# Performance work log

Measured on AMD Instinct MI355X. Metric: run time of the kernel, lower is better.

The kernel has to match this reference:

```python
import jax, jax.numpy as jnp
import numpy as np

B, T, N, E = 64, 500, 21, 210
IN_DIM, HID, OUT_DIM = 1, 128, 1


def gcn_norm(edge_index, edge_weight, num_nodes):
    # PyG gcn_norm: add self loops (weight 1), deg over target nodes, symmetric normalization.
    src, dst = edge_index[0], edge_index[1]
    loop = jnp.arange(num_nodes)
    src = jnp.concatenate([src, loop])
    dst = jnp.concatenate([dst, loop])
    ew = jnp.concatenate([edge_weight, jnp.ones((num_nodes,), edge_weight.dtype)])
    deg = jnp.zeros((num_nodes,), edge_weight.dtype).at[dst].add(ew)
    dinv = jnp.where(deg > 0, deg ** -0.5, 0.0)
    norm = dinv[src] * ew * dinv[dst]
    # Dense N x N (N=21, tiny) normalized adjacency; out[i] = sum_j A[i, j] x[j].
    return jnp.zeros((num_nodes, num_nodes), edge_weight.dtype).at[dst, src].add(norm)


def _forward(edge_index, x, edge_weight, Wz_1, bz_1, lzw_1, lzb_1, Wr_1, br_1, lrw_1, lrb_1, Wh_1, bh_1, lhw_1, lhb_1, Wz_2, bz_2, lzw_2, lzb_2, Wr_2, br_2, lrw_2, lrb_2, Wh_2, bh_2, lhw_2, lhb_2, cls_w, cls_b):
    A = gcn_norm(edge_index, edge_weight, N)

    def gcn(X, W, b):  # X: (B, N, F)
        return jnp.einsum("ij,bjf->bif", A, X @ W) + b

    def cell(X, H, Wz, bz, lzw, lzb, Wr, br, lrw, lrb, Wh, bh, lhw, lhb):
        Z = jax.nn.sigmoid(jnp.concatenate([gcn(X, Wz, bz), H], -1) @ lzw + lzb)
        R = jax.nn.sigmoid(jnp.concatenate([gcn(X, Wr, br), H], -1) @ lrw + lrb)
        Ht = jnp.tanh(jnp.concatenate([gcn(X, Wh, bh), H * R], -1) @ lhw + lhb)
        return Z * H + (1.0 - Z) * Ht

    def step(carry, x_t):  # x_t: (B, N)
        H1, H2 = carry
        X = x_t[..., None]  # (B, N, 1)
        H1 = cell(X, H1, Wz_1, bz_1, lzw_1, lzb_1, Wr_1, br_1, lrw_1, lrb_1, Wh_1, bh_1, lhw_1, lhb_1)
        H2 = cell(H1, H2, Wz_2, bz_2, lzw_2, lzb_2, Wr_2, br_2, lrw_2, lrb_2, Wh_2, bh_2, lhw_2, lhb_2)
        return (H1, H2), H2.mean(axis=1)  # mean over nodes -> (B, HID)

    H0 = jnp.zeros((x.shape[0], N, HID), x.dtype)
    _, outs = jax.lax.scan(step, (H0, H0), jnp.moveaxis(x, 1, 0))  # outs: (T, B, HID)
    seq_out = outs.mean(axis=0)  # mean over time (== mean over nodes then time in original)
    return seq_out @ cls_w + cls_b  # (B, OUT_DIM)


def setup_inputs():
    key = jax.random.key(0)
    ks = list(jax.random.split(key, 20))
    kit = iter(ks)

    def nrm(shape, scale=0.05):
        return jax.random.normal(next(kit), shape, jnp.float32) * scale

    inp = {}
    inp["x"] = jax.random.normal(next(kit), (B, T, N), jnp.float32)
    inp["edge_index"] = jax.random.randint(next(kit), (2, E), 0, N)
    inp["edge_weight"] = jax.random.uniform(next(kit), (E,), jnp.float32)
    for tag, in_dim in (("1", IN_DIM), ("2", HID)):
        for g in "zrh":
            inp[f"W{g}_{tag}"] = nrm((in_dim, HID))
            inp[f"b{g}_{tag}"] = jnp.zeros((HID,), jnp.float32)
            inp[f"l{g}w_{tag}"] = nrm((2 * HID, HID))
            inp[f"l{g}b_{tag}"] = jnp.zeros((HID,), jnp.float32)
    inp["cls_w"] = nrm((HID, OUT_DIM))
    inp["cls_b"] = jnp.zeros((OUT_DIM,), jnp.float32)
    return inp


def reference(x, edge_index, edge_weight, Wz_1, bz_1, lzw_1, lzb_1, Wr_1, br_1, lrw_1, lrb_1, Wh_1, bh_1, lhw_1, lhb_1, Wz_2, bz_2, lzw_2, lzb_2, Wr_2, br_2, lrw_2, lrb_2, Wh_2, bh_2, lhw_2, lhb_2, cls_w, cls_b):
    return _forward(edge_index, x, edge_weight, Wz_1, bz_1, lzw_1, lzb_1, Wr_1, br_1, lrw_1, lrb_1, Wh_1, bh_1, lhw_1, lhb_1, Wz_2, bz_2, lzw_2, lzb_2, Wr_2, br_2, lrw_2, lrb_2, Wh_2, bh_2, lhw_2, lhb_2, cls_w, cls_b)
```

## Files before the change

### kernel.cpp

```cpp
#include <hip/hip_runtime.h>
#include <hip/hip_bf16.h>


#define NN 21
#define NROW 24
#define HID 128
#define TSTEPS 500
#define EDGES 210
#define RPT 6

#define WS_A     0
#define WS_VEC   1600
#define WS_LZR1  3200
#define WS_LH1   36000
#define WS_WE2   52400
#define WS_LZR2  101600
#define WS_LH2   134400
#define WS_FLAGS 150784
#define WS_RING  154880
#define RING_SLOT 3072

#define WAVE_SYNC() asm volatile("s_waitcnt lgkmcnt(0)" ::: "memory")
#define VM_SYNC()   asm volatile("s_waitcnt vmcnt(0)" ::: "memory")

typedef float v2f __attribute__((ext_vector_type(2)));

__device__ __forceinline__ v2f lo2(float4 w) { v2f v = {w.x, w.y}; return v; }
__device__ __forceinline__ v2f hi2(float4 w) { v2f v = {w.z, w.w}; return v; }
__device__ __forceinline__ void pkf(v2f& acc, float s, v2f w) {
    v2f ss = {s, s};
    acc = __builtin_elementwise_fma(ss, w, acc);
}
__device__ __forceinline__ float sigmoidf(float v) {
    return 1.0f / (1.0f + expf(-v));
}
__device__ __forceinline__ void dc_store(float* p, float v) {
    asm volatile("global_store_dword %0, %1, off sc0 sc1" :: "v"(p), "v"(v) : "memory");
}

__global__ void build_A(const int* __restrict__ ei, const float* __restrict__ ew,
                        float* __restrict__ Aout) {
    __shared__ double deg[NN];
    __shared__ double dinv[NN];
    __shared__ double Asm[NN * NN];
    int t = threadIdx.x;
    for (int k = t; k < NN * NN; k += blockDim.x) Asm[k] = 0.0;
    if (t < NN) deg[t] = 1.0;
    __syncthreads();
    if (t == 0) {
        for (int e = 0; e < EDGES; e++) deg[ei[EDGES + e]] += (double)ew[e];
        for (int i = 0; i < NN; i++) dinv[i] = deg[i] > 0.0 ? 1.0 / sqrt(deg[i]) : 0.0;
        for (int e = 0; e < EDGES; e++) {
            int s = ei[e], d = ei[EDGES + e];
            Asm[d * NN + s] += dinv[s] * (double)ew[e] * dinv[d];
        }
        for (int i = 0; i < NN; i++) Asm[i * NN + i] += dinv[i] * dinv[i];
    }
    __syncthreads();
    for (int k = t; k < NROW * NN; k += blockDim.x)
        Aout[k] = (k < NN * NN) ? (float)Asm[k] : 0.0f;
}

// ... 41 lines not shown
    double a0 = 0, a1 = 0, a2 = 0, a3 = 0;
    for (int m = 0; m < 128; m++) {
        double w0 = (double)W[k * 128 + m];
        double w1 = (double)W[(k + 1) * 128 + m];
        a0 += w0 * (double)L[m * 128 + f0];
        a1 += w0 * (double)L[m * 128 + f0 + 64];
        a2 += w1 * (double)L[m * 128 + f0];
        a3 += w1 * (double)L[m * 128 + f0 + 64];
    }
    out[t] = make_float4((float)a0, (float)a1, (float)a2, (float)a3);
}

__global__ void make_vecs(const float* __restrict__ Wz1, const float* __restrict__ Wr1,
                          const float* __restrict__ Wh1,
                          const float* __restrict__ bz1, const float* __restrict__ br1,
                          const float* __restrict__ bh1,
                          const float* __restrict__ lzw1, const float* __restrict__ lrw1,
                          const float* __restrict__ lhw1,
                          const float* __restrict__ lzb1, const float* __restrict__ lrb1,
                          const float* __restrict__ lhb1,
                          const float* __restrict__ bz2, const float* __restrict__ br2,
                          const float* __restrict__ bh2,
                          const float* __restrict__ lzw2, const float* __restrict__ lrw2,
                          const float* __restrict__ lhw2,
                          const float* __restrict__ lzb2, const float* __restrict__ lrb2,
                          const float* __restrict__ lhb2,
                          float* __restrict__ out) {
    int t = blockIdx.x * blockDim.x + threadIdx.x;
    if (t >= 9 * 128) return;
    int v = t >> 7, f = t & 127;
    double acc = 0.0;
    if (v < 3) {
        const float* W = (v == 0) ? Wz1 : (v == 1) ? Wr1 : Wh1;
        const float* L = (v == 0) ? lzw1 : (v == 1) ? lrw1 : lhw1;
        for (int m = 0; m < 128; m++) acc += (double)W[m] * (double)L[m * 128 + f];
    } else if (v < 6) {
        int g = v - 3;
        const float* bb = (g == 0) ? bz1 : (g == 1) ? br1 : bh1;
        const float* L  = (g == 0) ? lzw1 : (g == 1) ? lrw1 : lhw1;
        const float* lb = (g == 0) ? lzb1 : (g == 1) ? lrb1 : lhb1;
        for (int m = 0; m < 128; m++) acc += (double)bb[m] * (double)L[m * 128 + f];
        acc += (double)lb[f];
    } else {
        int g = v - 6;
        const float* bb = (g == 0) ? bz2 : (g == 1) ? br2 : bh2;
        const float* L  = (g == 0) ? lzw2 : (g == 1) ? lrw2 : lhw2;
        const float* lb = (g == 0) ? lzb2 : (g == 1) ? lrb2 : lhb2;
        for (int m = 0; m < 128; m++) acc += (double)bb[m] * (double)L[m * 128 + f];
        acc += (double)lb[f];
    }
    out[t] = (float)acc;
}

__global__ __launch_bounds__(256, 1) void tgcn_split(
    const float* __restrict__ x, float* __restrict__ ws,
    const float* __restrict__ cls_w, const float* __restrict__ cls_b,
    float* __restrict__ out, int rdepth)
{
    const int bid = blockIdx.x;
    const bool roleA = (bid < 64);
    const int b  = bid & 63;
    const int t  = threadIdx.x;
    const int f0 = t & 63;
    const int f1 = f0 + 64;
    const int gw = __builtin_amdgcn_readfirstlane(t >> 6);
    const int iA = gw * RPT;
    const int nreal = (iA + RPT <= NN) ? RPT : (NN - iA);
    const int dmask = rdepth - 1;

    unsigned* fwdp  = (unsigned*)(ws + WS_FLAGS) + b * 32;
    unsigned* backp = (unsigned*)(ws + WS_FLAGS) + 2048 + b * 32;
    float* ringB = ws + WS_RING + (size_t)b * ((size_t)rdepth * RING_SLOT);

    __shared__ __align__(16) float sH1[2][NROW * HID];
    __shared__ __align__(16) float sHR1[NROW * HID];
    __shared__ __align__(16) float sH1B[2][NROW * HID];
    __shared__ __align__(16) float sH2[NROW * HID];
    __shared__ __align__(16) float sHR2[NROW * HID];
    __shared__ __align__(16) float sAH[NROW * HID];
    __shared__ float sA[NROW * NN];
    __shared__ float sax[2][NROW];
    __shared__ double sred[4][HID];

    const float*  vecs = ws + WS_VEC;
    const float4* Lzr1 = (const float4*)(ws + WS_LZR1);
    const float4* Lh1  = (const float4*)(ws + WS_LH1);
    const float4* We2  = (const float4*)(ws + WS_WE2);
    const float4* Lzr2 = (const float4*)(ws + WS_LZR2);
    const float4* Lh2  = (const float4*)(ws + WS_LH2);

    const float4* HR1v = (const float4*)sHR1;
    const float4* HR2v = (const float4*)sHR2;
    const float4* AHv  = (const float4*)sAH;
    const float4* H2v  = (const float4*)sH2;

    for (int k = t; k < 2 * NROW * HID; k += 256) {
        ((float*)sH1)[k] = 0.0f;
        ((float*)sH1B)[k] = 0.0f;
    }
    for (int k = t; k < NROW * HID; k += 256) {
        sH2[k] = 0.0f; sHR1[k] = 0.0f; sHR2[k] = 0.0f; sAH[k] = 0.0f;
    }
    for (int k = t; k < NROW * NN; k += 256) sA[k] = ws[WS_A + k];

    const v2f wz1v = {vecs[f0],        vecs[f1]};
    const v2f wr1v = {vecs[128 + f0],  vecs[128 + f1]};
    const v2f wh1v = {vecs[256 + f0],  vecs[256 + f1]};
    const v2f cz1v = {vecs[384 + f0],  vecs[384 + f1]};
    const v2f cr1v = {vecs[512 + f0],  vecs[512 + f1]};
    const v2f ch1v = {vecs[640 + f0],  vecs[640 + f1]};
    const v2f cz2v = {vecs[768 + f0],  vecs[768 + f1]};
    const v2f cr2v = {vecs[896 + f0],  vecs[896 + f1]};
    const v2f ch2v = {vecs[1024 + f0], vecs[1024 + f1]};

    __syncthreads();

    if (roleA) {
        const float* xb = x + (size_t)b * (TSTEPS * NN);
        if (t < NROW) {
            float a0s = 0.0f, a1s = 0.0f;
            for (int j = 0; j < NN; j++) {
                a0s = fmaf(sA[t * NN + j], xb[j], a0s);
                a1s = fmaf(sA[t * NN + j], xb[NN + j], a1s);
            }
            sax[0][t] = a0s;
            sax[1][t] = a1s;
        }
        __syncthreads();

        for (int s = 0; s < TSTEPS; s++) {
            if (t == 0 && s >= rdepth) {
                while (__hip_atomic_load(backp, __ATOMIC_RELAXED,
                                         __HIP_MEMORY_SCOPE_AGENT) < (unsigned)(s - rdepth + 1))
                    __builtin_amdgcn_s_sleep(2);
            }
            __syncthreads();

            {
                const float* H1rd = sH1[(s + 1) & 1];
                float*       H1wr = sH1[s & 1];
                const float4* H1c = (const float4*)H1rd;
                float* g = ringB + (s & dmask) * RING_SLOT;
                float axp[RPT];
                #pragma unroll
                for (int r = 0; r < RPT; r++) axp[r] = sax[s & 1][iA + r];
                v2f az[RPT], ar[RPT];
                #pragma unroll
                for (int r = 0; r < RPT; r++) {
                    az[r] = __builtin_elementwise_fma((v2f){axp[r], axp[r]}, wz1v, cz1v);
                    ar[r] = __builtin_elementwise_fma((v2f){axp[r], axp[r]}, wr1v, cr1v);
                }
                #pragma unroll 2
                for (int c = 0; c < 32; ++c) {
                    const float4 wz0 = Lzr1[c * 256 + f0];
                    const float4 wz1 = Lzr1[c * 256 + 64 + f0];
                    const float4 wr0 = Lzr1[c * 256 + 128 + f0];
                    const float4 wr1 = Lzr1[c * 256 + 192 + f0];
                    #pragma unroll
                    for (int r = 0; r < RPT; r++) {
                        const float4 h = H1c[(iA + r) * 32 + c];
                        pkf(az[r], h.x, lo2(wz0)); pkf(az[r], h.y, hi2(wz0));
                        pkf(az[r], h.z, lo2(wz1)); pkf(az[r], h.w, hi2(wz1));
                        pkf(ar[r], h.x, lo2(wr0)); pkf(ar[r], h.y, hi2(wr0));
                        pkf(ar[r], h.z, lo2(wr1)); pkf(ar[r], h.w, hi2(wr1));
                    }
                }
                v2f zg[RPT], h1c[RPT];
                #pragma unroll
                for (int r = 0; r < RPT; r++) {
                    zg[r].x = sigmoidf(az[r].x);
                    zg[r].y = sigmoidf(az[r].y);
                    const float r0 = sigmoidf(ar[r].x);
                    const float r1 = sigmoidf(ar[r].y);
                    h1c[r].x = H1rd[(iA + r) * HID + f0];
                    h1c[r].y = H1rd[(iA + r) * HID + f1];
                    sHR1[(iA + r) * HID + f0] = h1c[r].x * r0;
                    sHR1[(iA + r) * HID + f1] = h1c[r].y * r1;
                }
                WAVE_SYNC();
                v2f ah[RPT];
                #pragma unroll
                for (int r = 0; r < RPT; r++)
                    ah[r] = __builtin_elementwise_fma((v2f){axp[r], axp[r]}, wh1v, ch1v);
                #pragma unroll 2
                for (int c = 0; c < 32; ++c) {
                    const float4 wh0 = Lh1[c * 128 + f0];
                    const float4 wh1 = Lh1[c * 128 + 64 + f0];
                    #pragma unroll
                    for (int r = 0; r < RPT; r++) {
                        const float4 q = HR1v[(iA + r) * 32 + c];
                        pkf(ah[r], q.x, lo2(wh0)); pkf(ah[r], q.y, hi2(wh0));
                        pkf(ah[r], q.z, lo2(wh1)); pkf(ah[r], q.w, hi2(wh1));
                    }
                }
                #pragma unroll
                for (int r = 0; r < RPT; r++) {
                    const int row = iA + r;
                    const float n0 = fmaf(zg[r].x, h1c[r].x, (1.0f - zg[r].x) * tanhf(ah[r].x));
                    const float n1 = fmaf(zg[r].y, h1c[r].y, (1.0f - zg[r].y) * tanhf(ah[r].y));
                    H1wr[row * HID + f0] = n0;
                    H1wr[row * HID + f1] = n1;
                    dc_store(g + row * HID + f0, n0);
                    dc_store(g + row * HID + f1, n1);
                }
            }
            if (t < NROW && s + 2 < TSTEPS) {
                const float* xt = xb + (size_t)(s + 2) * NN;
                float a = 0.0f;
                for (int j = 0; j < NN; j++) a = fmaf(sA[t * NN + j], xt[j], a);
                sax[(s + 2) & 1][t] = a;
            }
            VM_SYNC();
            __syncthreads();
            if (t == 0)
                __hip_atomic_store(fwdp, (unsigned)(s + 1), __ATOMIC_RELAXED,
                                   __HIP_MEMORY_SCOPE_AGENT);
        }
        return;
    }

    double oacc0 = 0.0, oacc1 = 0.0;
    v2f ph[RPT], z2[RPT], h2c[RPT];

    auto l2_p5 = [&]() {
        #pragma unroll 2
        for (int c = 0; c < 32; ++c) {
            const float4 lh0 = Lh2[c * 128 + f0];
            const float4 lh1 = Lh2[c * 128 + 64 + f0];
            #pragma unroll
            for (int r = 0; r < RPT; r++) {
                const float4 q = HR2v[(iA + r) * 32 + c];
                pkf(ph[r], q.x, lo2(lh0)); pkf(ph[r], q.y, hi2(lh0));
                pkf(ph[r], q.z, lo2(lh1)); pkf(ph[r], q.w, hi2(lh1));
            }
        }
        #pragma unroll
        for (int r = 0; r < RPT; r++) {
            const float m0 = fmaf(z2[r].x, h2c[r].x, (1.0f - z2[r].x) * tanhf(ph[r].x));
            const float m1 = fmaf(z2[r].y, h2c[r].y, (1.0f - z2[r].y) * tanhf(ph[r].y));
            sH2[(iA + r) * HID + f0] = m0;
            sH2[(iA + r) * HID + f1] = m1;
            if (r < nreal) {
                oacc0 += (double)m0;
                oacc1 += (double)m1;
            }
        }
    };

    {
        if (t == 0) {
            while (__hip_atomic_load(fwdp, __ATOMIC_RELAXED,
                                     __HIP_MEMORY_SCOPE_AGENT) < 1u)
                __builtin_amdgcn_s_sleep(2);
        }
        __syncthreads();
        const float4* gs = (const float4*)(ringB + 0 * RING_SLOT);
        const float4* p0 = gs + t;
        const float4* p1 = gs + t + 256;
        const float4* p2 = gs + t + 512;
        float4 v0, v1, v2;
        asm volatile(
            "global_load_dwordx4 %0, %3, off sc0 sc1\n\t"
            "global_load_dwordx4 %1, %4, off sc0 sc1\n\t"
            "global_load_dwordx4 %2, %5, off sc0 sc1\n\t"
            "s_waitcnt vmcnt(0)"
            : "=v"(v0), "=v"(v1), "=v"(v2)
            : "v"(p0), "v"(p1), "v"(p2)
            : "memory");
        float4* sB = (float4*)sH1B[0];
        sB[t] = v0; sB[t + 256] = v1; sB[t + 512] = v2;
        __syncthreads();
        if (t == 0)
            __hip_atomic_store(backp, 1u, __ATOMIC_RELAXED,
                               __HIP_MEMORY_SCOPE_AGENT);
    }

    for (int k = 0; k < TSTEPS; k++) {
        const float* H1k = sH1B[k & 1];
        {
            v2f aa[RPT];
            #pragma unroll
            for (int r = 0; r < RPT; r++) aa[r] = (v2f){0.0f, 0.0f};
            #pragma unroll 3
            for (int j = 0; j < NN; j++) {
                const v2f hj = {H1k[j * HID + f0], H1k[j * HID + f1]};
                #pragma unroll
                for (int r = 0; r < RPT; r++) {
                    const float arj = sA[(iA + r) * NN + j];
                    aa[r] = __builtin_elementwise_fma((v2f){arj, arj}, hj, aa[r]);
                }
            }
            #pragma unroll
            for (int r = 0; r < RPT; r++) {
                sAH[(iA + r) * HID + f0] = aa[r].x;
                sAH[(iA + r) * HID + f1] = aa[r].y;
            }
        }
        WAVE_SYNC();
        const bool pf = (k + 1 < TSTEPS);
        float4 v0, v1, v2;
        if (pf) {
            if (t == 0) {
                while (__hip_atomic_load(fwdp, __ATOMIC_RELAXED,
                                         __HIP_MEMORY_SCOPE_AGENT) < (unsigned)(k + 2))
                    __builtin_amdgcn_s_sleep(2);
            }
            __syncthreads();
            const float4* gs = (const float4*)(ringB + ((k + 1) & dmask) * RING_SLOT);
            const float4* p0 = gs + t;
            const float4* p1 = gs + t + 256;
            const float4* p2 = gs + t + 512;
            asm volatile(
                "global_load_dwordx4 %0, %3, off sc0 sc1\n\t"
                "global_load_dwordx4 %1, %4, off sc0 sc1\n\t"
                "global_load_dwordx4 %2, %5, off sc0 sc1"
                : "=v"(v0), "=v"(v1), "=v"(v2)
                : "v"(p0), "v"(p1), "v"(p2)
                : "memory");
        }
        {
            v2f pz[RPT], pr[RPT];
            #pragma unroll
            for (int r = 0; r < RPT; r++) { pz[r] = cz2v; pr[r] = cr2v; ph[r] = ch2v; }
            for (int c = 0; c < 32; ++c) {
                const float4 wz0 = We2[c * 384 + f0];
                const float4 wz1 = We2[c * 384 + 64 + f0];
                const float4 wr0 = We2[c * 384 + 128 + f0];
                const float4 wr1 = We2[c * 384 + 192 + f0];
                const float4 wh0 = We2[c * 384 + 256 + f0];
                const float4 wh1 = We2[c * 384 + 320 + f0];
                const float4 lz0 = Lzr2[c * 256 + f0];
                const float4 lz1 = Lzr2[c * 256 + 64 + f0];
                const float4 lr0 = Lzr2[c * 256 + 128 + f0];
                const float4 lr1 = Lzr2[c * 256 + 192 + f0];
                #pragma unroll
                for (int r = 0; r < RPT; r++) {
                    const float4 a = AHv[(iA + r) * 32 + c];
                    const float4 q = H2v[(iA + r) * 32 + c];
                    pkf(pz[r], a.x, lo2(wz0)); pkf(pz[r], a.y, hi2(wz0));
                    pkf(pz[r], a.z, lo2(wz1)); pkf(pz[r], a.w, hi2(wz1));
                    pkf(pz[r], q.x, lo2(lz0)); pkf(pz[r], q.y, hi2(lz0));
                    pkf(pz[r], q.z, lo2(lz1)); pkf(pz[r], q.w, hi2(lz1));
                    pkf(pr[r], a.x, lo2(wr0)); pkf(pr[r], a.y, hi2(wr0));
                    pkf(pr[r], a.z, lo2(wr1)); pkf(pr[r], a.w, hi2(wr1));
                    pkf(pr[r], q.x, lo2(lr0)); pkf(pr[r], q.y, hi2(lr0));
                    pkf(pr[r], q.z, lo2(lr1)); pkf(pr[r], q.w, hi2(lr1));
                    pkf(ph[r], a.x, lo2(wh0)); pkf(ph[r], a.y, hi2(wh0));
                    pkf(ph[r], a.z, lo2(wh1)); pkf(ph[r], a.w, hi2(wh1));
                }
            }
            #pragma unroll
            for (int r = 0; r < RPT; r++) {
                z2[r].x = sigmoidf(pz[r].x);
                z2[r].y = sigmoidf(pz[r].y);
                const float r20 = sigmoidf(pr[r].x);
                const float r21 = sigmoidf(pr[r].y);
                h2c[r].x = sH2[(iA + r) * HID + f0];
                h2c[r].y = sH2[(iA + r) * HID + f1];
                sHR2[(iA + r) * HID + f0] = h2c[r].x * r20;
                sHR2[(iA + r) * HID + f1] = h2c[r].y * r21;
            }
        }
        WAVE_SYNC();
        if (pf) {
            asm volatile("s_waitcnt vmcnt(0)" ::: "memory");
            __builtin_amdgcn_sched_barrier(0);
            float4* sB = (float4*)sH1B[(k + 1) & 1];
            sB[t] = v0; sB[t + 256] = v1; sB[t + 512] = v2;
            __syncthreads();
            if (t == 0)
                __hip_atomic_store(backp, (unsigned)(k + 2), __ATOMIC_RELAXED,
                                   __HIP_MEMORY_SCOPE_AGENT);
        }
        l2_p5();
    }

    sred[gw][f0] = oacc0;
    sred[gw][f1] = oacc1;
    __syncthreads();
    if (t < HID) {
        double s = 0.0;
        for (int gg = 0; gg < 4; gg++) s += sred[gg][t];
        sred[0][t] = (s / (double)(TSTEPS * NN)) * (double)cls_w[t];
    }
    __syncthreads();
    if (t < 64) {
        double v = ((double*)sred)[t] + ((double*)sred)[t + 64];
        for (int off = 32; off; off >>= 1) v += __shfl_down(v, off, 64);
        if (t == 0) out[b] = (float)(v + (double)cls_b[0]);
    }
}

#define NTHREADS 512
__global__ __launch_bounds__(NTHREADS, 1) void tgcn_main(
    const float* __restrict__ x, const float* __restrict__ ws,
    const float* __restrict__ cls_w, const float* __restrict__ cls_b,
    float* __restrict__ out)
{
    const int b  = blockIdx.x;
    const int t  = threadIdx.x;
    const bool isA = (t < 256);
    const int lt = t & 255;
    const int f0 = lt & 63;
    const int f1 = f0 + 64;
    const int gw = __builtin_amdgcn_readfirstlane(lt >> 6);
    const int iA = gw * RPT;
    const int nreal = (iA + RPT <= NN) ? RPT : (NN - iA);

    __shared__ __align__(16) float sH1[2][NROW * HID];
    __shared__ __align__(16) float sH2[NROW * HID];
    __shared__ __align__(16) float sHR1[NROW * HID];
    __shared__ __align__(16) float sHR2[NROW * HID];
    __shared__ __align__(16) float sAH[NROW * HID];
    __shared__ float sA[NROW * NN];
    __shared__ float sax[2][NROW];
    __shared__ double sred[4][HID];

    const float*  vecs = ws + WS_VEC;
    const float4* Lzr1 = (const float4*)(ws + WS_LZR1);
    const float4* Lh1  = (const float4*)(ws + WS_LH1);
    const float4* We2  = (const float4*)(ws + WS_WE2);
    const float4* Lzr2 = (const float4*)(ws + WS_LZR2);
    const float4* Lh2  = (const float4*)(ws + WS_LH2);

    const float4* H2v  = (const float4*)sH2;
    const float4* HR1v = (const float4*)sHR1;
    const float4* HR2v = (const float4*)sHR2;
    const float4* AHv  = (const float4*)sAH;

    for (int k = t; k < 2 * NROW * HID; k += NTHREADS) ((float*)sH1)[k] = 0.0f;
    for (int k = t; k < NROW * HID; k += NTHREADS) sH2[k] = 0.0f;
    for (int k = t; k < NROW * NN; k += NTHREADS) sA[k] = ws[WS_A + k];

    const v2f wz1v = {vecs[f0],        vecs[f1]};
    const v2f wr1v = {vecs[128 + f0],  vecs[128 + f1]};
    const v2f wh1v = {vecs[256 + f0],  vecs[256 + f1]};
// ... 212 lines not shown
    const float* x    = (const float*)d_in[0];
    const int*   ei   = (const int*)  d_in[1];
    const float* ew   = (const float*)d_in[2];
    const float* Wz1  = (const float*)d_in[3];
    const float* bz1  = (const float*)d_in[4];
    const float* lzw1 = (const float*)d_in[5];
    const float* lzb1 = (const float*)d_in[6];
    const float* Wr1  = (const float*)d_in[7];
    const float* br1  = (const float*)d_in[8];
    const float* lrw1 = (const float*)d_in[9];
    const float* lrb1 = (const float*)d_in[10];
    const float* Wh1  = (const float*)d_in[11];
    const float* bh1  = (const float*)d_in[12];
    const float* lhw1 = (const float*)d_in[13];
    const float* lhb1 = (const float*)d_in[14];
    const float* Wz2  = (const float*)d_in[15];
    const float* bz2  = (const float*)d_in[16];
    const float* lzw2 = (const float*)d_in[17];
    const float* lzb2 = (const float*)d_in[18];
    const float* Wr2  = (const float*)d_in[19];
    const float* br2  = (const float*)d_in[20];
    const float* lrw2 = (const float*)d_in[21];
    const float* lrb2 = (const float*)d_in[22];
    const float* Wh2  = (const float*)d_in[23];
    const float* bh2  = (const float*)d_in[24];
    const float* lhw2 = (const float*)d_in[25];
    const float* lhb2 = (const float*)d_in[26];
    const float* clsw = (const float*)d_in[27];
    const float* clsb = (const float*)d_in[28];

    float* ws   = (float*)d_ws;
    float* outp = (float*)d_out;

    build_A<<<1, 64, 0, stream>>>(ei, ew, ws + WS_A);
    pack_bot<<<32, 256, 0, stream>>>(lzw1, lrw1, (float4*)(ws + WS_LZR1), 2);
    pack_bot<<<16, 256, 0, stream>>>(lhw1, lhw1, (float4*)(ws + WS_LH1), 1);
    pack_bot<<<32, 256, 0, stream>>>(lzw2, lrw2, (float4*)(ws + WS_LZR2), 2);
    pack_bot<<<16, 256, 0, stream>>>(lhw2, lhw2, (float4*)(ws + WS_LH2), 1);
    make_weff2<<<48, 256, 0, stream>>>(Wz2, Wr2, Wh2, lzw2, lrw2, lhw2,
                                       (float4*)(ws + WS_WE2));
    make_vecs<<<5, 256, 0, stream>>>(Wz1, Wr1, Wh1, bz1, br1, bh1,
                                     lzw1, lrw1, lhw1, lzb1, lrb1, lhb1,
                                     bz2, br2, bh2, lzw2, lrw2, lhw2,
                                     lzb2, lrb2, lhb2, ws + WS_VEC);

    const size_t need4 = (size_t)(WS_RING + 64 * 4 * RING_SLOT) * sizeof(float);
    const size_t need2 = (size_t)(WS_RING + 64 * 2 * RING_SLOT) * sizeof(float);
    int rdepth = 0;
    if (ws_size >= need4)      rdepth = 4;
    else if (ws_size >= need2) rdepth = 2;

    if (rdepth) {
        init_flags<<<16, 256, 0, stream>>>((unsigned*)(ws + WS_FLAGS));
        tgcn_split<<<128, 256, 0, stream>>>(x, ws, clsw, clsb, outp, rdepth);
    } else {
        tgcn_main<<<64, NTHREADS, 0, stream>>>(x, ws, clsw, clsb, outp);
    }
}
```

Measured before the change: 10.06 ms.

## Double split-kernel block size to 512 threads with 3 rows per thread

Raises tgcn_split from 256 to 512 threads per block. Each wave now splits its lanes into two row groups of 3 rows, and each wave covers half of the feature columns, so every thread works on 3 node rows instead of 6. The goal is more parallelism per CU and shorter per-thread serial FMA chains for the recurrent step. The cost is extra block-wide __syncthreads barriers, since cross-wave LDS data dependencies now exist, plus a shuffle-based final reduction and reworked ring-buffer loads.

After: 12.66 ms. +25.9%, slower.

```diff
diff --git a/kernel.cpp b/kernel.cpp
--- a/kernel.cpp
+++ b/kernel.cpp
@@ -8,6 +8,7 @@
 #define TSTEPS 500
 #define EDGES 210
 #define RPT 6
+#define RPTS 3
 
 #define WS_A     0
 #define WS_VEC   1600
@@ -155,7 +156,7 @@
     out[t] = (float)acc;
 }
 
-__global__ __launch_bounds__(256, 1) void tgcn_split(
+__global__ __launch_bounds__(512, 1) void tgcn_split(
     const float* __restrict__ x, float* __restrict__ ws,
     const float* __restrict__ cls_w, const float* __restrict__ cls_b,
     float* __restrict__ out, int rdepth)
@@ -164,11 +165,15 @@
     const bool roleA = (bid < 64);
     const int b  = bid & 63;
     const int t  = threadIdx.x;
-    const int f0 = t & 63;
+    const int w  = __builtin_amdgcn_readfirstlane(t >> 6);
+    const int lane = t & 63;
+    const int half = w & 1;
+    const int wp = w >> 1;
+    const int rg = wp * 2 + (lane >> 5);
+    const int iA = rg * RPTS;
+    const int f0 = (lane & 31) + half * 32;
     const int f1 = f0 + 64;
-    const int gw = __builtin_amdgcn_readfirstlane(t >> 6);
-    const int iA = gw * RPT;
-    const int nreal = (iA + RPT <= NN) ? RPT : (NN - iA);
+    const int nreal = (iA + RPTS <= NN) ? RPTS : ((NN > iA) ? (NN - iA) : 0);
     const int dmask = rdepth - 1;
 
     unsigned* fwdp  = (unsigned*)(ws + WS_FLAGS) + b * 32;
@@ -197,14 +202,14 @@
     const float4* AHv  = (const float4*)sAH;
     const float4* H2v  = (const float4*)sH2;
 
-    for (int k = t; k < 2 * NROW * HID; k += 256) {
+    for (int k = t; k < 2 * NROW * HID; k += 512) {
         ((float*)sH1)[k] = 0.0f;
         ((float*)sH1B)[k] = 0.0f;
     }
-    for (int k = t; k < NROW * HID; k += 256) {
+    for (int k = t; k < NROW * HID; k += 512) {
         sH2[k] = 0.0f; sHR1[k] = 0.0f; sHR2[k] = 0.0f; sAH[k] = 0.0f;
     }
-    for (int k = t; k < NROW * NN; k += 256) sA[k] = ws[WS_A + k];
+    for (int k = t; k < NROW * NN; k += 512) sA[k] = ws[WS_A + k];
 
     const v2f wz1v = {vecs[f0],        vecs[f1]};
     const v2f wr1v = {vecs[128 + f0],  vecs[128 + f1]};
@@ -244,12 +249,12 @@
                 float*       H1wr = sH1[s & 1];
                 const float4* H1c = (const float4*)H1rd;
                 float* g = ringB + (s & dmask) * RING_SLOT;
-                float axp[RPT];
-                #pragma unroll
-                for (int r = 0; r < RPT; r++) axp[r] = sax[s & 1][iA + r];
-                v2f az[RPT], ar[RPT];
-                #pragma unroll
-                for (int r = 0; r < RPT; r++) {
+                float axp[RPTS];
+                #pragma unroll
+                for (int r = 0; r < RPTS; r++) axp[r] = sax[s & 1][iA + r];
+                v2f az[RPTS], ar[RPTS];
+                #pragma unroll
+                for (int r = 0; r < RPTS; r++) {
                     az[r] = __builtin_elementwise_fma((v2f){axp[r], axp[r]}, wz1v, cz1v);
                     ar[r] = __builtin_elementwise_fma((v2f){axp[r], axp[r]}, wr1v, cr1v);
                 }
@@ -260,7 +265,7 @@
                     const float4 wr0 = Lzr1[c * 256 + 128 + f0];
                     const float4 wr1 = Lzr1[c * 256 + 192 + f0];
                     #pragma unroll
-                    for (int r = 0; r < RPT; r++) {
+                    for (int r = 0; r < RPTS; r++) {
                         const float4 h = H1c[(iA + r) * 32 + c];
                         pkf(az[r], h.x, lo2(wz0)); pkf(az[r], h.y, hi2(wz0));
                         pkf(az[r], h.z, lo2(wz1)); pkf(az[r], h.w, hi2(wz1));
@@ -268,9 +273,9 @@
                         pkf(ar[r], h.z, lo2(wr1)); pkf(ar[r], h.w, hi2(wr1));
                     }
                 }
-                v2f zg[RPT], h1c[RPT];
-                #pragma unroll
-                for (int r = 0; r < RPT; r++) {
+                v2f zg[RPTS], h1c[RPTS];
+                #pragma unroll
+                for (int r = 0; r < RPTS; r++) {
                     zg[r].x = sigmoidf(az[r].x);
                     zg[r].y = sigmoidf(az[r].y);
                     const float r0 = sigmoidf(ar[r].x);
@@ -281,23 +286,24 @@
                     sHR1[(iA + r) * HID + f1] = h1c[r].y * r1;
                 }
                 WAVE_SYNC();
-                v2f ah[RPT];
-                #pragma unroll
-                for (int r = 0; r < RPT; r++)
+                __syncthreads();
+                v2f ah[RPTS];
+                #pragma unroll
+                for (int r = 0; r < RPTS; r++)
                     ah[r] = __builtin_elementwise_fma((v2f){axp[r], axp[r]}, wh1v, ch1v);
                 #pragma unroll 2
                 for (int c = 0; c < 32; ++c) {
                     const float4 wh0 = Lh1[c * 128 + f0];
                     const float4 wh1 = Lh1[c * 128 + 64 + f0];
                     #pragma unroll
-                    for (int r = 0; r < RPT; r++) {
+                    for (int r = 0; r < RPTS; r++) {
                         const float4 q = HR1v[(iA + r) * 32 + c];
                         pkf(ah[r], q.x, lo2(wh0)); pkf(ah[r], q.y, hi2(wh0));
                         pkf(ah[r], q.z, lo2(wh1)); pkf(ah[r], q.w, hi2(wh1));
                     }
                 }
                 #pragma unroll
-                for (int r = 0; r < RPT; r++) {
+                for (int r = 0; r < RPTS; r++) {
                     const int row = iA + r;
                     const float n0 = fmaf(zg[r].x, h1c[r].x, (1.0f - zg[r].x) * tanhf(ah[r].x));
                     const float n1 = fmaf(zg[r].y, h1c[r].y, (1.0f - zg[r].y) * tanhf(ah[r].y));
@@ -323,7 +329,7 @@
     }
 
     double oacc0 = 0.0, oacc1 = 0.0;
-    v2f ph[RPT], z2[RPT], h2c[RPT];
+    v2f ph[RPTS], z2[RPTS], h2c[RPTS];
 
     auto l2_p5 = [&]() {
         #pragma unroll 2
@@ -331,14 +337,14 @@
             const float4 lh0 = Lh2[c * 128 + f0];
             const float4 lh1 = Lh2[c * 128 + 64 + f0];
             #pragma unroll
-            for (int r = 0; r < RPT; r++) {
+            for (int r = 0; r < RPTS; r++) {
                 const float4 q = HR2v[(iA + r) * 32 + c];
                 pkf(ph[r], q.x, lo2(lh0)); pkf(ph[r], q.y, hi2(lh0));
                 pkf(ph[r], q.z, lo2(lh1)); pkf(ph[r], q.w, hi2(lh1));
             }
         }
         #pragma unroll
-        for (int r = 0; r < RPT; r++) {
+        for (int r = 0; r < RPTS; r++) {
             const float m0 = fmaf(z2[r].x, h2c[r].x, (1.0f - z2[r].x) * tanhf(ph[r].x));
             const float m1 = fmaf(z2[r].y, h2c[r].y, (1.0f - z2[r].y) * tanhf(ph[r].y));
             sH2[(iA + r) * HID + f0] = m0;
@@ -358,20 +364,22 @@
         }
         __syncthreads();
         const float4* gs = (const float4*)(ringB + 0 * RING_SLOT);
-        const float4* p0 = gs + t;
-        const float4* p1 = gs + t + 256;
-        const float4* p2 = gs + t + 512;
-        float4 v0, v1, v2;
-        asm volatile(
-            "global_load_dwordx4 %0, %3, off sc0 sc1\n\t"
-            "global_load_dwordx4 %1, %4, off sc0 sc1\n\t"
-            "global_load_dwordx4 %2, %5, off sc0 sc1\n\t"
-            "s_waitcnt vmcnt(0)"
-            : "=v"(v0), "=v"(v1), "=v"(v2)
-            : "v"(p0), "v"(p1), "v"(p2)
-            : "memory");
+        float4 v0, v1;
+        {
+            const float4* p0 = gs + t;
+            asm volatile("global_load_dwordx4 %0, %1, off sc0 sc1"
+                         : "=v"(v0) : "v"(p0) : "memory");
+        }
+        if (t < 256) {
+            const float4* p1 = gs + t + 512;
+            asm volatile("global_load_dwordx4 %0, %1, off sc0 sc1"
+                         : "=v"(v1) : "v"(p1) : "memory");
+        }
+        asm volatile("s_waitcnt vmcnt(0)" ::: "memory");
+        __builtin_amdgcn_sched_barrier(0);
         float4* sB = (float4*)sH1B[0];
-        sB[t] = v0; sB[t + 256] = v1; sB[t + 512] = v2;
+        sB[t] = v0;
+        if (t < 256) sB[t + 512] = v1;
         __syncthreads();
         if (t == 0)
             __hip_atomic_store(backp, 1u, __ATOMIC_RELAXED,
@@ -381,27 +389,28 @@
     for (int k = 0; k < TSTEPS; k++) {
         const float* H1k = sH1B[k & 1];
         {
-            v2f aa[RPT];
-            #pragma unroll
-            for (int r = 0; r < RPT; r++) aa[r] = (v2f){0.0f, 0.0f};
+            v2f aa[RPTS];
+            #pragma unroll
+            for (int r = 0; r < RPTS; r++) aa[r] = (v2f){0.0f, 0.0f};
             #pragma unroll 3
             for (int j = 0; j < NN; j++) {
                 const v2f hj = {H1k[j * HID + f0], H1k[j * HID + f1]};
                 #pragma unroll
-                for (int r = 0; r < RPT; r++) {
+                for (int r = 0; r < RPTS; r++) {
                     const float arj = sA[(iA + r) * NN + j];
                     aa[r] = __builtin_elementwise_fma((v2f){arj, arj}, hj, aa[r]);
                 }
             }
             #pragma unroll
-            for (int r = 0; r < RPT; r++) {
+            for (int r = 0; r < RPTS; r++) {
                 sAH[(iA + r) * HID + f0] = aa[r].x;
                 sAH[(iA + r) * HID + f1] = aa[r].y;
             }
         }
         WAVE_SYNC();
+        __syncthreads();
         const bool pf = (k + 1 < TSTEPS);
-        float4 v0, v1, v2;
+        float4 v0, v1;
         if (pf) {
             if (t == 0) {
                 while (__hip_atomic_load(fwdp, __ATOMIC_RELAXED,
@@ -410,21 +419,21 @@
             }
             __syncthreads();
             const float4* gs = (const float4*)(ringB + ((k + 1) & dmask) * RING_SLOT);
-            const float4* p0 = gs + t;
-            const float4* p1 = gs + t + 256;
-            const float4* p2 = gs + t + 512;
-            asm volatile(
-                "global_load_dwordx4 %0, %3, off sc0 sc1\n\t"
-                "global_load_dwordx4 %1, %4, off sc0 sc1\n\t"
-                "global_load_dwordx4 %2, %5, off sc0 sc1"
-                : "=v"(v0), "=v"(v1), "=v"(v2)
-                : "v"(p0), "v"(p1), "v"(p2)
-                : "memory");
+            {
+                const float4* p0 = gs + t;
+                asm volatile("global_load_dwordx4 %0, %1, off sc0 sc1"
+                             : "=v"(v0) : "v"(p0) : "memory");
+            }
+            if (t < 256) {
+                const float4* p1 = gs + t + 512;
+                asm volatile("global_load_dwordx4 %0, %1, off sc0 sc1"
+                             : "=v"(v1) : "v"(p1) : "memory");
+            }
         }
         {
-            v2f pz[RPT], pr[RPT];
-            #pragma unroll
-            for (int r = 0; r < RPT; r++) { pz[r] = cz2v; pr[r] = cr2v; ph[r] = ch2v; }
+            v2f pz[RPTS], pr[RPTS];
+            #pragma unroll
+            for (int r = 0; r < RPTS; r++) { pz[r] = cz2v; pr[r] = cr2v; ph[r] = ch2v; }
             for (int c = 0; c < 32; ++c) {
                 const float4 wz0 = We2[c * 384 + f0];
                 const float4 wz1 = We2[c * 384 + 64 + f0];
@@ -437,7 +446,7 @@
                 const float4 lr0 = Lzr2[c * 256 + 128 + f0];
                 const float4 lr1 = Lzr2[c * 256 + 192 + f0];
                 #pragma unroll
-                for (int r = 0; r < RPT; r++) {
+                for (int r = 0; r < RPTS; r++) {
                     const float4 a = AHv[(iA + r) * 32 + c];
                     const float4 q = H2v[(iA + r) * 32 + c];
                     pkf(pz[r], a.x, lo2(wz0)); pkf(pz[r], a.y, hi2(wz0));
@@ -453,7 +462,7 @@
                 }
             }
             #pragma unroll
-            for (int r = 0; r < RPT; r++) {
+            for (int r = 0; r < RPTS; r++) {
                 z2[r].x = sigmoidf(pz[r].x);
                 z2[r].y = sigmoidf(pz[r].y);
                 const float r20 = sigmoidf(pr[r].x);
@@ -465,21 +474,31 @@
             }
         }
         WAVE_SYNC();
+        __syncthreads();
         if (pf) {
             asm volatile("s_waitcnt vmcnt(0)" ::: "memory");
             __builtin_amdgcn_sched_barrier(0);
             float4* sB = (float4*)sH1B[(k + 1) & 1];
-            sB[t] = v0; sB[t + 256] = v1; sB[t + 512] = v2;
+            sB[t] = v0;
+            if (t < 256) sB[t + 512] = v1;
             __syncthreads();
             if (t == 0)
                 __hip_atomic_store(backp, (unsigned)(k + 2), __ATOMIC_RELAXED,
                                    __HIP_MEMORY_SCOPE_AGENT);
         }
         l2_p5();
-    }
-
-    sred[gw][f0] = oacc0;
-    sred[gw][f1] = oacc1;
+        __syncthreads();
+    }
+
+    {
+        double v0 = oacc0, v1 = oacc1;
+        v0 += __shfl_down(v0, 32, 64);
+        v1 += __shfl_down(v1, 32, 64);
+        if ((lane >> 5) == 0) {
+            sred[wp][f0] = v0;
+            sred[wp][f1] = v1;
+        }
+    }
     __syncthreads();
     if (t < HID) {
         double s = 0.0;
@@ -803,7 +822,7 @@
 
     if (rdepth) {
         init_flags<<<16, 256, 0, stream>>>((unsigned*)(ws + WS_FLAGS));
-        tgcn_split<<<128, 256, 0, stream>>>(x, ws, clsw, clsb, outp, rdepth);
+        tgcn_split<<<128, 512, 0, stream>>>(x, ws, clsw, clsb, outp, rdepth);
     } else {
         tgcn_main<<<64, NTHREADS, 0, stream>>>(x, ws, clsw, clsb, outp);
     }
```

## Split GRU gate matmuls across waves by gate instead of by node rows

Applied to the files above, without the earlier changes.

Within each 4-wave block, work is now partitioned by gate: two waves compute the Z gate over 12 rows each while the other two compute R, with results exchanged through new shared buffers (sZG, sZ2) and block-wide barriers. This halves weight loads per wave per gate and doubles row reuse of each loaded weight. In the layer-2 role, the waves that finish R then do the ring-buffer prefetch and wait on the forward flag, while the Z waves compute the candidate state, so the flag wait and global loads overlap with compute. It adds more __syncthreads per step and extra shared memory, and the candidate-state phase runs on only two waves.

New measurement: 28.63 ms. 185% more time.

```diff
diff --git a/kernel.cpp b/kernel.cpp
--- a/kernel.cpp
+++ b/kernel.cpp
@@ -164,11 +164,10 @@
     const bool roleA = (bid < 64);
     const int b  = bid & 63;
     const int t  = threadIdx.x;
-    const int f0 = t & 63;
+    const int w  = __builtin_amdgcn_readfirstlane(t >> 6);
+    const int lane = t & 63;
+    const int f0 = lane;
     const int f1 = f0 + 64;
-    const int gw = __builtin_amdgcn_readfirstlane(t >> 6);
-    const int iA = gw * RPT;
-    const int nreal = (iA + RPT <= NN) ? RPT : (NN - iA);
     const int dmask = rdepth - 1;
 
     unsigned* fwdp  = (unsigned*)(ws + WS_FLAGS) + b * 32;
@@ -177,13 +176,15 @@
 
     __shared__ __align__(16) float sH1[2][NROW * HID];
     __shared__ __align__(16) float sHR1[NROW * HID];
+    __shared__ __align__(16) float sZG[NROW * HID];
     __shared__ __align__(16) float sH1B[2][NROW * HID];
     __shared__ __align__(16) float sH2[NROW * HID];
     __shared__ __align__(16) float sHR2[NROW * HID];
     __shared__ __align__(16) float sAH[NROW * HID];
+    __shared__ __align__(16) float sZ2[NROW * HID];
     __shared__ float sA[NROW * NN];
     __shared__ float sax[2][NROW];
-    __shared__ double sred[4][HID];
+    __shared__ double sred[2][HID];
 
     const float*  vecs = ws + WS_VEC;
     const float4* Lzr1 = (const float4*)(ws + WS_LZR1);
@@ -203,6 +204,7 @@
     }
     for (int k = t; k < NROW * HID; k += 256) {
         sH2[k] = 0.0f; sHR1[k] = 0.0f; sHR2[k] = 0.0f; sAH[k] = 0.0f;
+        sZG[k] = 0.0f; sZ2[k] = 0.0f;
     }
     for (int k = t; k < NROW * NN; k += 256) sA[k] = ws[WS_A + k];
 
@@ -239,68 +241,94 @@
             }
             __syncthreads();
 
-            {
-                const float* H1rd = sH1[(s + 1) & 1];
-                float*       H1wr = sH1[s & 1];
-                const float4* H1c = (const float4*)H1rd;
-                float* g = ringB + (s & dmask) * RING_SLOT;
-                float axp[RPT];
-                #pragma unroll
-                for (int r = 0; r < RPT; r++) axp[r] = sax[s & 1][iA + r];
-                v2f az[RPT], ar[RPT];
-                #pragma unroll
-                for (int r = 0; r < RPT; r++) {
-                    az[r] = __builtin_elementwise_fma((v2f){axp[r], axp[r]}, wz1v, cz1v);
-                    ar[r] = __builtin_elementwise_fma((v2f){axp[r], axp[r]}, wr1v, cr1v);
+            const float* H1rd = sH1[(s + 1) & 1];
+            float*       H1wr = sH1[s & 1];
+            const float4* H1c = (const float4*)H1rd;
+            float* g = ringB + (s & dmask) * RING_SLOT;
+
+            if (w < 2) {
+                const int base = w * 12;
+                v2f az[12];
+                #pragma unroll
+                for (int r = 0; r < 12; r++) {
+                    const float ax = sax[s & 1][base + r];
+                    az[r] = __builtin_elementwise_fma((v2f){ax, ax}, wz1v, cz1v);
                 }
                 #pragma unroll 2
                 for (int c = 0; c < 32; ++c) {
                     const float4 wz0 = Lzr1[c * 256 + f0];
                     const float4 wz1 = Lzr1[c * 256 + 64 + f0];
+                    #pragma unroll
+                    for (int r = 0; r < 12; r++) {
+                        const float4 h = H1c[(base + r) * 32 + c];
+                        pkf(az[r], h.x, lo2(wz0)); pkf(az[r], h.y, hi2(wz0));
+                        pkf(az[r], h.z, lo2(wz1)); pkf(az[r], h.w, hi2(wz1));
+                    }
+                }
+                #pragma unroll
+                for (int r = 0; r < 12; r++) {
+                    const int row = base + r;
+                    sZG[row * HID + f0] = sigmoidf(az[r].x);
+                    sZG[row * HID + f1] = sigmoidf(az[r].y);
+                }
+            } else {
+                const int base = (w - 2) * 12;
+                v2f ar[12];
+                #pragma unroll
+                for (int r = 0; r < 12; r++) {
+                    const float ax = sax[s & 1][base + r];
+                    ar[r] = __builtin_elementwise_fma((v2f){ax, ax}, wr1v, cr1v);
+                }
+                #pragma unroll 2
+                for (int c = 0; c < 32; ++c) {
                     const float4 wr0 = Lzr1[c * 256 + 128 + f0];
                     const float4 wr1 = Lzr1[c * 256 + 192 + f0];
                     #pragma unroll
-                    for (int r = 0; r < RPT; r++) {
-                        const float4 h = H1c[(iA + r) * 32 + c];
-                        pkf(az[r], h.x, lo2(wz0)); pkf(az[r], h.y, hi2(wz0));
-                        pkf(az[r], h.z, lo2(wz1)); pkf(az[r], h.w, hi2(wz1));
+                    for (int r = 0; r < 12; r++) {
+                        const float4 h = H1c[(base + r) * 32 + c];
                         pkf(ar[r], h.x, lo2(wr0)); pkf(ar[r], h.y, hi2(wr0));
                         pkf(ar[r], h.z, lo2(wr1)); pkf(ar[r], h.w, hi2(wr1));
                     }
                 }
-                v2f zg[RPT], h1c[RPT];
-                #pragma unroll
-                for (int r = 0; r < RPT; r++) {
-                    zg[r].x = sigmoidf(az[r].x);
-                    zg[r].y = sigmoidf(az[r].y);
+                #pragma unroll
+                for (int r = 0; r < 12; r++) {
+                    const int row = base + r;
                     const float r0 = sigmoidf(ar[r].x);
                     const float r1 = sigmoidf(ar[r].y);
-                    h1c[r].x = H1rd[(iA + r) * HID + f0];
-                    h1c[r].y = H1rd[(iA + r) * HID + f1];
-                    sHR1[(iA + r) * HID + f0] = h1c[r].x * r0;
-                    sHR1[(iA + r) * HID + f1] = h1c[r].y * r1;
-                }
-                WAVE_SYNC();
-                v2f ah[RPT];
-                #pragma unroll
-                for (int r = 0; r < RPT; r++)
-                    ah[r] = __builtin_elementwise_fma((v2f){axp[r], axp[r]}, wh1v, ch1v);
+                    sHR1[row * HID + f0] = H1rd[row * HID + f0] * r0;
+                    sHR1[row * HID + f1] = H1rd[row * HID + f1] * r1;
+                }
+            }
+            __syncthreads();
+
+            {
+                const int base = w * 6;
+                v2f ah[6];
+                #pragma unroll
+                for (int r = 0; r < 6; r++) {
+                    const float ax = sax[s & 1][base + r];
+                    ah[r] = __builtin_elementwise_fma((v2f){ax, ax}, wh1v, ch1v);
+                }
                 #pragma unroll 2
                 for (int c = 0; c < 32; ++c) {
                     const float4 wh0 = Lh1[c * 128 + f0];
                     const float4 wh1 = Lh1[c * 128 + 64 + f0];
                     #pragma unroll
-                    for (int r = 0; r < RPT; r++) {
-                        const float4 q = HR1v[(iA + r) * 32 + c];
+                    for (int r = 0; r < 6; r++) {
+                        const float4 q = HR1v[(base + r) * 32 + c];
                         pkf(ah[r], q.x, lo2(wh0)); pkf(ah[r], q.y, hi2(wh0));
                         pkf(ah[r], q.z, lo2(wh1)); pkf(ah[r], q.w, hi2(wh1));
                     }
                 }
                 #pragma unroll
-                for (int r = 0; r < RPT; r++) {
-                    const int row = iA + r;
-                    const float n0 = fmaf(zg[r].x, h1c[r].x, (1.0f - zg[r].x) * tanhf(ah[r].x));
-                    const float n1 = fmaf(zg[r].y, h1c[r].y, (1.0f - zg[r].y) * tanhf(ah[r].y));
+                for (int r = 0; r < 6; r++) {
+                    const int row = base + r;
+                    const float zg0 = sZG[row * HID + f0];
+                    const float zg1 = sZG[row * HID + f1];
+                    const float h10 = H1rd[row * HID + f0];
+                    const float h11 = H1rd[row * HID + f1];
+                    const float n0 = fmaf(zg0, h10, (1.0f - zg0) * tanhf(ah[r].x));
+                    const float n1 = fmaf(zg1, h11, (1.0f - zg1) * tanhf(ah[r].y));
                     H1wr[row * HID + f0] = n0;
                     H1wr[row * HID + f1] = n1;
                     dc_store(g + row * HID + f0, n0);
@@ -323,32 +351,6 @@
     }
 
     double oacc0 = 0.0, oacc1 = 0.0;
-    v2f ph[RPT], z2[RPT], h2c[RPT];
-
-    auto l2_p5 = [&]() {
-        #pragma unroll 2
-        for (int c = 0; c < 32; ++c) {
-            const float4 lh0 = Lh2[c * 128 + f0];
-            const float4 lh1 = Lh2[c * 128 + 64 + f0];
-            #pragma unroll
-            for (int r = 0; r < RPT; r++) {
-                const float4 q = HR2v[(iA + r) * 32 + c];
-                pkf(ph[r], q.x, lo2(lh0)); pkf(ph[r], q.y, hi2(lh0));
-                pkf(ph[r], q.z, lo2(lh1)); pkf(ph[r], q.w, hi2(lh1));
-            }
-        }
-        #pragma unroll
-        for (int r = 0; r < RPT; r++) {
-            const float m0 = fmaf(z2[r].x, h2c[r].x, (1.0f - z2[r].x) * tanhf(ph[r].x));
-            const float m1 = fmaf(z2[r].y, h2c[r].y, (1.0f - z2[r].y) * tanhf(ph[r].y));
-            sH2[(iA + r) * HID + f0] = m0;
-            sH2[(iA + r) * HID + f1] = m1;
-            if (r < nreal) {
-                oacc0 += (double)m0;
-                oacc1 += (double)m1;
-            }
-        }
-    };
 
     {
         if (t == 0) {
@@ -370,6 +372,7 @@
             : "=v"(v0), "=v"(v1), "=v"(v2)
             : "v"(p0), "v"(p1), "v"(p2)
             : "memory");
+        __builtin_amdgcn_sched_barrier(0);
         float4* sB = (float4*)sH1B[0];
         sB[t] = v0; sB[t + 256] = v1; sB[t + 512] = v2;
         __syncthreads();
@@ -381,110 +384,174 @@
     for (int k = 0; k < TSTEPS; k++) {
         const float* H1k = sH1B[k & 1];
         {
-            v2f aa[RPT];
-            #pragma unroll
-            for (int r = 0; r < RPT; r++) aa[r] = (v2f){0.0f, 0.0f};
+            const int base = w * 6;
+            v2f aa[6];
+            #pragma unroll
+            for (int r = 0; r < 6; r++) aa[r] = (v2f){0.0f, 0.0f};
             #pragma unroll 3
             for (int j = 0; j < NN; j++) {
                 const v2f hj = {H1k[j * HID + f0], H1k[j * HID + f1]};
                 #pragma unroll
-                for (int r = 0; r < RPT; r++) {
-                    const float arj = sA[(iA + r) * NN + j];
+                for (int r = 0; r < 6; r++) {
+                    const float arj = sA[(base + r) * NN + j];
                     aa[r] = __builtin_elementwise_fma((v2f){arj, arj}, hj, aa[r]);
                 }
             }
             #pragma unroll
-            for (int r = 0; r < RPT; r++) {
-                sAH[(iA + r) * HID + f0] = aa[r].x;
-                sAH[(iA + r) * HID + f1] = aa[r].y;
-            }
-        }
-        WAVE_SYNC();
-        const bool pf = (k + 1 < TSTEPS);
-        float4 v0, v1, v2;
-        if (pf) {
-            if (t == 0) {
-                while (__hip_atomic_load(fwdp, __ATOMIC_RELAXED,
-                                         __HIP_MEMORY_SCOPE_AGENT) < (unsigned)(k + 2))
-                    __builtin_amdgcn_s_sleep(2);
-            }
-            __syncthreads();
-            const float4* gs = (const float4*)(ringB + ((k + 1) & dmask) * RING_SLOT);
-            const float4* p0 = gs + t;
-            const float4* p1 = gs + t + 256;
-            const float4* p2 = gs + t + 512;
-            asm volatile(
-                "global_load_dwordx4 %0, %3, off sc0 sc1\n\t"
-                "global_load_dwordx4 %1, %4, off sc0 sc1\n\t"
-                "global_load_dwordx4 %2, %5, off sc0 sc1"
-                : "=v"(v0), "=v"(v1), "=v"(v2)
-                : "v"(p0), "v"(p1), "v"(p2)
-                : "memory");
-        }
-        {
-            v2f pz[RPT], pr[RPT];
-            #pragma unroll
-            for (int r = 0; r < RPT; r++) { pz[r] = cz2v; pr[r] = cr2v; ph[r] = ch2v; }
+            for (int r = 0; r < 6; r++) {
+                sAH[(base + r) * HID + f0] = aa[r].x;
+                sAH[(base + r) * HID + f1] = aa[r].y;
+            }
+        }
+        __syncthreads();
+
+        if (w < 2) {
+            const int base = w * 12;
+            v2f pz[12];
+            #pragma unroll
+            for (int r = 0; r < 12; r++) pz[r] = cz2v;
+            #pragma unroll 2
             for (int c = 0; c < 32; ++c) {
                 const float4 wz0 = We2[c * 384 + f0];
                 const float4 wz1 = We2[c * 384 + 64 + f0];
-                const float4 wr0 = We2[c * 384 + 128 + f0];
-                const float4 wr1 = We2[c * 384 + 192 + f0];
-                const float4 wh0 = We2[c * 384 + 256 + f0];
-                const float4 wh1 = We2[c * 384 + 320 + f0];
                 const float4 lz0 = Lzr2[c * 256 + f0];
                 const float4 lz1 = Lzr2[c * 256 + 64 + f0];
-                const float4 lr0 = Lzr2[c * 256 + 128 + f0];
-                const float4 lr1 = Lzr2[c * 256 + 192 + f0];
-                #pragma unroll
-                for (int r = 0; r < RPT; r++) {
-                    const float4 a = AHv[(iA + r) * 32 + c];
-                    const float4 q = H2v[(iA + r) * 32 + c];
+                #pragma unroll
+                for (int r = 0; r < 12; r++) {
+                    const float4 a = AHv[(base + r) * 32 + c];
+                    const float4 q = H2v[(base + r) * 32 + c];
                     pkf(pz[r], a.x, lo2(wz0)); pkf(pz[r], a.y, hi2(wz0));
                     pkf(pz[r], a.z, lo2(wz1)); pkf(pz[r], a.w, hi2(wz1));
                     pkf(pz[r], q.x, lo2(lz0)); pkf(pz[r], q.y, hi2(lz0));
                     pkf(pz[r], q.z, lo2(lz1)); pkf(pz[r], q.w, hi2(lz1));
+                }
+            }
+            #pragma unroll
+            for (int r = 0; r < 12; r++) {
+                const int row = base + r;
+                sZ2[row * HID + f0] = sigmoidf(pz[r].x);
+                sZ2[row * HID + f1] = sigmoidf(pz[r].y);
+            }
+        } else {
+            const int base = (w - 2) * 12;
+            v2f pr[12];
+            #pragma unroll
+            for (int r = 0; r < 12; r++) pr[r] = cr2v;
+            #pragma unroll 2
+            for (int c = 0; c < 32; ++c) {
+                const float4 wr0 = We2[c * 384 + 128 + f0];
+                const float4 wr1 = We2[c * 384 + 192 + f0];
+                const float4 lr0 = Lzr2[c * 256 + 128 + f0];
+                const float4 lr1 = Lzr2[c * 256 + 192 + f0];
+                #pragma unroll
+                for (int r = 0; r < 12; r++) {
+                    const float4 a = AHv[(base + r) * 32 + c];
+                    const float4 q = H2v[(base + r) * 32 + c];
                     pkf(pr[r], a.x, lo2(wr0)); pkf(pr[r], a.y, hi2(wr0));
                     pkf(pr[r], a.z, lo2(wr1)); pkf(pr[r], a.w, hi2(wr1));
                     pkf(pr[r], q.x, lo2(lr0)); pkf(pr[r], q.y, hi2(lr0));
                     pkf(pr[r], q.z, lo2(lr1)); pkf(pr[r], q.w, hi2(lr1));
+                }
+            }
+            #pragma unroll
+            for (int r = 0; r < 12; r++) {
+                const int row = base + r;
+                const float r20 = sigmoidf(pr[r].x);
+                const float r21 = sigmoidf(pr[r].y);
+                sHR2[row * HID + f0] = sH2[row * HID + f0] * r20;
+                sHR2[row * HID + f1] = sH2[row * HID + f1] * r21;
+            }
+        }
+        __syncthreads();
+
+        const bool pf = (k + 1 < TSTEPS);
+        if (w >= 2) {
+            if (pf) {
+                while (__hip_atomic_load(fwdp, __ATOMIC_RELAXED,
+                                         __HIP_MEMORY_SCOPE_AGENT) < (unsigned)(k + 2))
+                    __builtin_amdgcn_s_sleep(2);
+                const float4* gs = (const float4*)(ringB + ((k + 1) & dmask) * RING_SLOT);
+                const int li = t - 128;
+                const float4* p0 = gs + li;
+                const float4* p1 = gs + li + 128;
+                const float4* p2 = gs + li + 256;
+                const float4* p3 = gs + li + 384;
+                const float4* p4 = gs + li + 512;
+                const float4* p5 = gs + li + 640;
+                float4 u0, u1, u2, u3, u4, u5;
+                asm volatile(
+                    "global_load_dwordx4 %0, %6, off sc0 sc1\n\t"
+                    "global_load_dwordx4 %1, %7, off sc0 sc1\n\t"
+                    "global_load_dwordx4 %2, %8, off sc0 sc1\n\t"
+                    "global_load_dwordx4 %3, %9, off sc0 sc1\n\t"
+                    "global_load_dwordx4 %4, %10, off sc0 sc1\n\t"
+                    "global_load_dwordx4 %5, %11, off sc0 sc1\n\t"
+                    "s_waitcnt vmcnt(0)"
+                    : "=v"(u0), "=v"(u1), "=v"(u2), "=v"(u3), "=v"(u4), "=v"(u5)
+                    : "v"(p0), "v"(p1), "v"(p2), "v"(p3), "v"(p4), "v"(p5)
+                    : "memory");
+                __builtin_amdgcn_sched_barrier(0);
+                float4* sB = (float4*)sH1B[(k + 1) & 1];
+                sB[li] = u0;        sB[li + 128] = u1;  sB[li + 256] = u2;
+                sB[li + 384] = u3;  sB[li + 512] = u4;  sB[li + 640] = u5;
+            }
+        } else {
+            const int base = w * 12;
+            v2f ph[12];
+            #pragma unroll
+            for (int r = 0; r < 12; r++) ph[r] = ch2v;
+            #pragma unroll 2
+            for (int c = 0; c < 32; ++c) {
+                const float4 wh0 = We2[c * 384 + 256 + f0];
+                const float4 wh1 = We2[c * 384 + 320 + f0];
+                #pragma unroll
+                for (int r = 0; r < 12; r++) {
+                    const float4 a = AHv[(base + r) * 32 + c];
                     pkf(ph[r], a.x, lo2(wh0)); pkf(ph[r], a.y, hi2(wh0));
                     pkf(ph[r], a.z, lo2(wh1)); pkf(ph[r], a.w, hi2(wh1));
                 }
             }
-            #pragma unroll
-            for (int r = 0; r < RPT; r++) {
-                z2[r].x = sigmoidf(pz[r].x);
-                z2[r].y = sigmoidf(pz[r].y);
-                const float r20 = sigmoidf(pr[r].x);
-                const float r21 = sigmoidf(pr[r].y);
-                h2c[r].x = sH2[(iA + r) * HID + f0];
-                h2c[r].y = sH2[(iA + r) * HID + f1];
-                sHR2[(iA + r) * HID + f0] = h2c[r].x * r20;
-                sHR2[(iA + r) * HID + f1] = h2c[r].y * r21;
-            }
-        }
-        WAVE_SYNC();
-        if (pf) {
-            asm volatile("s_waitcnt vmcnt(0)" ::: "memory");
-            __builtin_amdgcn_sched_barrier(0);
-            float4* sB = (float4*)sH1B[(k + 1) & 1];
-            sB[t] = v0; sB[t + 256] = v1; sB[t + 512] = v2;
-            __syncthreads();
-            if (t == 0)
-                __hip_atomic_store(backp, (unsigned)(k + 2), __ATOMIC_RELAXED,
-                                   __HIP_MEMORY_SCOPE_AGENT);
-        }
-        l2_p5();
-    }
-
-    sred[gw][f0] = oacc0;
-    sred[gw][f1] = oacc1;
+            #pragma unroll 2
+            for (int c = 0; c < 32; ++c) {
+                const float4 lh0 = Lh2[c * 128 + f0];
+                const float4 lh1 = Lh2[c * 128 + 64 + f0];
+                #pragma unroll
+                for (int r = 0; r < 12; r++) {
+                    const float4 q = HR2v[(base + r) * 32 + c];
+                    pkf(ph[r], q.x, lo2(lh0)); pkf(ph[r], q.y, hi2(lh0));
+                    pkf(ph[r], q.z, lo2(lh1)); pkf(ph[r], q.w, hi2(lh1));
+                }
+            }
+            #pragma unroll
+            for (int r = 0; r < 12; r++) {
+                const int row = base + r;
+                const float z20 = sZ2[row * HID + f0];
+                const float z21 = sZ2[row * HID + f1];
+                const float h20 = sH2[row * HID + f0];
+                const float h21 = sH2[row * HID + f1];
+                const float m0 = fmaf(z20, h20, (1.0f - z20) * tanhf(ph[r].x));
+                const float m1 = fmaf(z21, h21, (1.0f - z21) * tanhf(ph[r].y));
+                sH2[row * HID + f0] = m0;
+                sH2[row * HID + f1] = m1;
+                if (row < NN) {
+                    oacc0 += (double)m0;
+                    oacc1 += (double)m1;
+                }
+            }
+        }
+        __syncthreads();
+        if (t == 0 && pf)
+            __hip_atomic_store(backp, (unsigned)(k + 2), __ATOMIC_RELAXED,
+                               __HIP_MEMORY_SCOPE_AGENT);
+    }
+
+    if (w < 2) {
+        sred[w][f0] = oacc0;
+        sred[w][f1] = oacc1;
+    }
     __syncthreads();
     if (t < HID) {
-        double s = 0.0;
-        for (int gg = 0; gg < 4; gg++) s += sred[gg][t];
-        sred[0][t] = (s / (double)(TSTEPS * NN)) * (double)cls_w[t];
+        sred[0][t] = ((sred[0][t] + sred[1][t]) / (double)(TSTEPS * NN)) * (double)cls_w[t];
     }
     __syncthreads();
     if (t < 64) {
```
